# Kernel optimization log

Measured on AMD Instinct MI355X. Metric: run time of the kernel, lower is better.

Reference implementation:

```python
import jax, jax.numpy as jnp
import numpy as np

B, S, D, H, HD, I, L = 1, 2048, 1024, 16, 64, 2816, 2
EPS = 1e-5
ROPE_BASE = 10000.0


def rmsnorm(x, w):
    return x * jax.lax.rsqrt(jnp.mean(x * x, axis=-1, keepdims=True) + EPS) * w


def precompute_freqs_cis():
    # matches precompute_freqs_cis: [S, HD//2, 2] = (cos, sin)
    freqs = 1.0 / (ROPE_BASE ** (jnp.arange(0, HD, 2, dtype=jnp.float32) / HD))
    ang = jnp.outer(jnp.arange(S, dtype=jnp.float32), freqs)
    return jnp.stack([jnp.cos(ang), jnp.sin(ang)], axis=-1)


def apply_rope(x, fc):
    # x: [B,S,H,HD]; fc: [S,HD//2,2] -> interleaved pair rotation
    xs = x.reshape(*x.shape[:-1], HD // 2, 2)
    f = fc[None, :, None]  # [1,S,1,HD//2,2]
    out = jnp.stack([
        xs[..., 0] * f[..., 0] - xs[..., 1] * f[..., 1],
        xs[..., 1] * f[..., 0] + xs[..., 0] * f[..., 1],
    ], axis=-1)
    return out.reshape(x.shape)


def setup_inputs() -> dict:
    key = jax.random.key(0)
    ks = jax.random.split(key, 6)
    p = lambda k, shape: jax.random.normal(k, shape, jnp.float32) * 0.02
    return {
        "x": jax.random.normal(ks[0], (B, S, D), jnp.float32),
        "wqkv": p(ks[1], (L, 3 * H * HD, D)),
        "wo": p(ks[2], (L, D, H * HD)),
        "w1": p(ks[3], (L, I, D)),
        "w2": p(ks[4], (L, D, I)),
        "w3": p(ks[5], (L, I, D)),
        "attn_norm_w": jnp.ones((L, D), jnp.float32),
        "ffn_norm_w": jnp.ones((L, D), jnp.float32),
        "attn_ls": 0.01 * jnp.ones((L, D), jnp.float32),
        "ffn_ls": 0.01 * jnp.ones((L, D), jnp.float32),
        "final_norm_w": jnp.ones((D,), jnp.float32),
    }


def reference(x, wqkv, wo, w1, w2, w3, attn_norm_w, ffn_norm_w, attn_ls, ffn_ls, final_norm_w):
    fc = precompute_freqs_cis()
    causal = jnp.tril(jnp.ones((S, S), dtype=bool))  # [S,S]
    scale = 1.0 / np.sqrt(HD).astype(np.float32)
    h = x
    for l in range(L):
        # --- attention block ---
        xn = rmsnorm(h, attn_norm_w[l])
        qkv = xn @ wqkv[l].T  # [B,S,3*H*HD]
        q, k, v = jnp.split(qkv, 3, axis=-1)
        q = apply_rope(q.reshape(B, S, H, HD), fc)
        k = apply_rope(k.reshape(B, S, H, HD), fc)
        v = v.reshape(B, S, H, HD)
        scores = jnp.einsum('bqhd,bkhd->bhqk', q, k) * scale
        scores = jnp.where(causal, scores, jnp.finfo(scores.dtype).min)
        attn = jax.nn.softmax(scores, axis=-1)
        y = jnp.einsum('bhqk,bkhd->bqhd', attn, v).reshape(B, S, H * HD)
        h = h + (y @ wo[l].T) * attn_ls[l]
        # --- feed-forward block (SwiGLU) ---
        xn = rmsnorm(h, ffn_norm_w[l])
        ff = (jax.nn.silu(xn @ w1[l].T) * (xn @ w3[l].T)) @ w2[l].T
        h = h + ff * ffn_ls[l]
    return rmsnorm(h, final_norm_w)
```

## Files before the change

### kernel.cpp

```cpp
#include <hip/hip_runtime.h>
#include <math.h>

#define SEQ 2048
#define DIM 1024
#define NH 16
#define HDIM 64
#define IDIM 2816
#define NL 2

typedef __attribute__((ext_vector_type(8))) short bf16x8;
typedef __attribute__((ext_vector_type(4))) float f32x4;

__device__ __forceinline__ unsigned short f2bf(float f) {
    unsigned int u = __float_as_uint(f);
    u = (u + 0x7fffu + ((u >> 16) & 1u)) >> 16;
    return (unsigned short)u;
}
__device__ __forceinline__ float bf2f(unsigned short u) {
    return __uint_as_float((unsigned int)u << 16);
}

__device__ __forceinline__ void gl_lds16(const void* g, void* l) {
    __builtin_amdgcn_global_load_lds(
        (const __attribute__((address_space(1))) unsigned int*)g,
        (__attribute__((address_space(3))) unsigned int*)l, 16, 0, 0);
}

#define WAITVM(n) asm volatile("s_waitcnt vmcnt(" #n ")" ::: "memory")
#define BARRIER_PIN()                       \
    do {                                    \
        __builtin_amdgcn_s_barrier();       \
        __builtin_amdgcn_sched_barrier(0);  \
    } while (0)

template <bool BF16OUT>
__global__ __launch_bounds__(256) void rmsnorm_kernel(const float* __restrict__ in,
                                                      const float* __restrict__ w,
                                                      void* __restrict__ out) {
    const int row = blockIdx.x;
    const int t = threadIdx.x;
    const float4 v = ((const float4*)(in + (size_t)row * DIM))[t];
    float ss = v.x * v.x + v.y * v.y + v.z * v.z + v.w * v.w;
#pragma unroll
    for (int m = 1; m < 64; m <<= 1) ss += __shfl_xor(ss, m);
    __shared__ float red[4];
    if ((t & 63) == 0) red[t >> 6] = ss;
    __syncthreads();
    const float tot = red[0] + red[1] + red[2] + red[3];
    const float r = 1.0f / sqrtf(tot * (1.0f / DIM) + 1e-5f);
    const float4 wv = ((const float4*)w)[t];
    float o0 = v.x * r * wv.x, o1 = v.y * r * wv.y;
    float o2 = v.z * r * wv.z, o3 = v.w * r * wv.w;
    if (BF16OUT) {
        ushort4 o = {f2bf(o0), f2bf(o1), f2bf(o2), f2bf(o3)};
        ((ushort4*)((unsigned short*)out + (size_t)row * DIM))[t] = o;
    } else {
        float4 o = {o0, o1, o2, o3};
        ((float4*)((float*)out + (size_t)row * DIM))[t] = o;
    }
}

#define WQKV_OFF 0
#define WO_OFF   3145728
#define W1_OFF   4194304
#define W3_OFF   7077888
#define W2_OFF   9961472
#define WTOT     12845056

__global__ __launch_bounds__(256) void convert_weights_kernel(
    const float* __restrict__ wqkv, const float* __restrict__ wo,
    const float* __restrict__ w1, const float* __restrict__ w3,
    const float* __restrict__ w2, unsigned short* __restrict__ out) {
    const size_t i8 = ((size_t)blockIdx.x * 256 + threadIdx.x) * 8;
    const float* src;
    size_t local;
    if (i8 < WO_OFF)      { src = wqkv; local = i8 - WQKV_OFF; }
    else if (i8 < W1_OFF) { src = wo;   local = i8 - WO_OFF; }
    else if (i8 < W3_OFF) { src = w1;   local = i8 - W1_OFF; }
    else if (i8 < W2_OFF) { src = w3;   local = i8 - W3_OFF; }
    else                  { src = w2;   local = i8 - W2_OFF; }
    const float4 v0 = *(const float4*)(src + local);
    const float4 v1 = *(const float4*)(src + local + 4);
    ushort4 o0 = {f2bf(v0.x), f2bf(v0.y), f2bf(v0.z), f2bf(v0.w)};
    ushort4 o1 = {f2bf(v1.x), f2bf(v1.y), f2bf(v1.z), f2bf(v1.w)};
    *(ushort4*)(out + i8) = o0;
    *(ushort4*)(out + i8 + 4) = o1;
}

template <int EPI, int BM, int BN, int KSPLIT>
__global__ __launch_bounds__(256) void mfma_gemm(
    const unsigned short* __restrict__ A,
    const unsigned short* __restrict__ B,
    const unsigned short* __restrict__ Bhi, int nsplit,
    float* __restrict__ Cf,
    unsigned short* __restrict__ Cb,
    const float* __restrict__ ls,
    int N, int K) {
    constexpr int MI = BM / 32;
    constexpr int NJ = BN / 32;
    constexpr int L = (BM + BN) / 32;
    static_assert(L == 6 || L == 8, "WAITVM literals cover L=6,8");
    __shared__ unsigned short As[2][BM * 64];
    __shared__ unsigned short Bs[2][BN * 64];

    const int tid = threadIdx.x;

    const int nwg = gridDim.x * gridDim.y;
    const int orig = blockIdx.y * gridDim.x + blockIdx.x;
    const int swz = (orig & 7) * (nwg >> 3) + (orig >> 3);
    const int bx = swz % gridDim.x;
    const int by = swz / gridDim.x;
    const int m0 = by * BM;
    const int ncol0 = bx * BN;

    const unsigned short* Bp = B;
    int n0 = ncol0;
    if (n0 >= nsplit) { Bp = Bhi; n0 -= nsplit; }

    const int Koff = (KSPLIT > 1) ? blockIdx.z * (K / KSPLIT) : 0;

    const int r0 = tid >> 3;
    const int cswz = (tid & 7) ^ (r0 & 7);
    const unsigned short* Ag = A + (size_t)(m0 + r0) * K + Koff + cswz * 8;
    const unsigned short* Bg = Bp + (size_t)(n0 + r0) * K + Koff + cswz * 8;

    const int lane = tid & 63;
    const int wid = tid >> 6;
    const int wr = (wid >> 1) * (BM / 2);
    const int wc = (wid & 1) * (BN / 2);
    const int fr = lane & 15;
    const int hi = lane >> 4;

    f32x4 acc[MI][NJ] = {};

    auto stage = [&](int buf, int kk) {
#pragma unroll
        for (int q = 0; q < BM / 32; ++q)
            gl_lds16(Ag + (size_t)(q * 32) * K + kk, &As[buf][q * 2048 + tid * 8]);
#pragma unroll
        for (int q = 0; q < BN / 32; ++q)
            gl_lds16(Bg + (size_t)(q * 32) * K + kk, &Bs[buf][q * 2048 + tid * 8]);
    };

    auto frag = [&](const unsigned short* base, int R, int c) -> bf16x8 {
        return *(const bf16x8*)&base[R * 64 + ((c ^ (R & 7)) << 3)];
    };

    auto compute_tile = [&](int buf) {
        bf16x8 a[MI][2], b[NJ][2];
#pragma unroll
        for (int m = 0; m < MI; ++m)
#pragma unroll
            for (int kw = 0; kw < 2; ++kw)
                a[m][kw] = frag(As[buf], wr + m * 16 + fr, kw * 4 + hi);
#pragma unroll
        for (int n = 0; n < NJ; ++n)
#pragma unroll
            for (int kw = 0; kw < 2; ++kw)
                b[n][kw] = frag(Bs[buf], wc + n * 16 + fr, kw * 4 + hi);
        __builtin_amdgcn_s_setprio(1);
#pragma unroll
        for (int kw = 0; kw < 2; ++kw)
#pragma unroll
            for (int m = 0; m < MI; ++m)
#pragma unroll
                for (int n = 0; n < NJ; ++n)
                    acc[m][n] = __builtin_amdgcn_mfma_f32_16x16x32_bf16(
                        a[m][kw], b[n][kw], acc[m][n], 0, 0, 0);
        __builtin_amdgcn_s_setprio(0);
    };

    const int NT = K / KSPLIT / 64;

    stage(0, 0);
    stage(1, 64);

    int buf = 0;
    for (int t = 0; t < NT - 1; ++t) {
        if constexpr (L == 6) WAITVM(6); else WAITVM(8);
        BARRIER_PIN();
        compute_tile(buf);
        asm volatile("s_waitcnt lgkmcnt(0)" ::: "memory");
        BARRIER_PIN();
        if (t + 2 < NT) stage(buf, (t + 2) * 64);
        buf ^= 1;
    }
    WAITVM(0);
    BARRIER_PIN();
    compute_tile(buf);

    const int erow = m0 + wr + hi * 4;
    const int ecol = ncol0 + wc + fr;
#pragma unroll
    for (int m = 0; m < MI; ++m) {
#pragma unroll
        for (int n = 0; n < NJ; ++n) {
            const f32x4 v = acc[m][n];
            const int row = erow + m * 16;
            const int col = ecol + n * 16;
            if (EPI == 1) {
                const float lv = ls[col];
#pragma unroll
                for (int j = 0; j < 4; ++j) {
                    float* p = Cf + (size_t)(row + j) * N + col;
                    if (KSPLIT > 1) atomicAdd(p, v[j] * lv);
                    else            *p = *p + v[j] * lv;
                }
            } else {
#pragma unroll
                for (int j = 0; j < 4; ++j)
                    Cb[(size_t)(row + j) * N + col] = f2bf(v[j]);
            }
        }
    }
}

__global__ __launch_bounds__(256) void silu_mul_kernel(
    const unsigned short* __restrict__ c13,
    unsigned short* __restrict__ outp) {
    const size_t e8 = ((size_t)blockIdx.x * 256 + threadIdx.x) * 8;
    const int m = (int)(e8 / IDIM);
    const int i = (int)(e8 % IDIM);
    const unsigned short* g = c13 + (size_t)m * (2 * IDIM) + i;
    const bf16x8 gv = *(const bf16x8*)g;
    const bf16x8 uv = *(const bf16x8*)(g + IDIM);
    unsigned short o[8];
#pragma unroll
    for (int j = 0; j < 8; ++j) {
        const float x = bf2f((unsigned short)gv[j]);
        const float u = bf2f((unsigned short)uv[j]);
        o[j] = f2bf(x / (1.0f + __expf(-x)) * u);
    }
    *(bf16x8*)(outp + (size_t)m * IDIM + i) = *(const bf16x8*)o;
}

__global__ __launch_bounds__(256) void rope_split_kernel(
    const unsigned short* __restrict__ qkv,
    unsigned short* __restrict__ Qh,
    unsigned short* __restrict__ Kh,
    unsigned short* __restrict__ Vt) {
    const int st = blockIdx.x;
    const int h = blockIdx.y;
    const int tid = threadIdx.x;
    const int srow = tid >> 2;
    const int scol = (tid & 3) * 16;
    const int s = st * 64 + srow;
    __shared__ unsigned short Vl[64][72];

    const unsigned short* base = qkv + (size_t)s * (3 * DIM) + h * HDIM + scol;

    unsigned short qv[16], kv[16], vv[16];
    *(bf16x8*)&qv[0] = *(const bf16x8*)(base);
    *(bf16x8*)&qv[8] = *(const bf16x8*)(base + 8);
    *(bf16x8*)&kv[0] = *(const bf16x8*)(base + DIM);
    *(bf16x8*)&kv[8] = *(const bf16x8*)(base + DIM + 8);
    *(bf16x8*)&vv[0] = *(const bf16x8*)(base + 2 * DIM);
    *(bf16x8*)&vv[8] = *(const bf16x8*)(base + 2 * DIM + 8);

    unsigned short qo[16], ko[16];
#pragma unroll
    for (int i = 0; i < 8; ++i) {
        const int p = scol / 2 + i;
        const float freq = powf(10000.0f, -(float)(2 * p) * (1.0f / 64.0f));
        const float ang = (float)s * freq;
        float sn, cs;
        sincosf(ang, &sn, &cs);
        const float q0 = bf2f(qv[2 * i]), q1 = bf2f(qv[2 * i + 1]);
        const float k0 = bf2f(kv[2 * i]), k1 = bf2f(kv[2 * i + 1]);
        qo[2 * i]     = f2bf(q0 * cs - q1 * sn);
        qo[2 * i + 1] = f2bf(q1 * cs + q0 * sn);
        ko[2 * i]     = f2bf(k0 * cs - k1 * sn);
        ko[2 * i + 1] = f2bf(k1 * cs + k0 * sn);
    }
    unsigned short* qdst = Qh + ((size_t)h * SEQ + s) * HDIM + scol;
    unsigned short* kdst = Kh + ((size_t)h * SEQ + s) * HDIM + scol;
    *(bf16x8*)qdst = *(const bf16x8*)&qo[0];
    *(bf16x8*)(qdst + 8) = *(const bf16x8*)&qo[8];
    *(bf16x8*)kdst = *(const bf16x8*)&ko[0];
    *(bf16x8*)(kdst + 8) = *(const bf16x8*)&ko[8];

#pragma unroll
    for (int i = 0; i < 16; ++i) Vl[scol + i][srow] = vv[i];
    __syncthreads();
    const int d = tid >> 2;
    const int c0 = (tid & 3) * 16;
    unsigned short* vdst = Vt + ((size_t)h * HDIM + d) * SEQ + st * 64 + c0;
    *(bf16x8*)vdst = *(const bf16x8*)&Vl[d][c0];
    *(bf16x8*)(vdst + 8) = *(const bf16x8*)&Vl[d][c0 + 8];
}

__global__ __launch_bounds__(256) void attn_mfma_kernel(
    const unsigned short* __restrict__ Qh,
    const unsigned short* __restrict__ Kh,
    const unsigned short* __restrict__ Vt,
    unsigned short* __restrict__ y) {
    const int h = blockIdx.x;
    const int qt = blockIdx.y;
    const int qb = (qt < 16) ? qt : 47 - qt;

    __shared__ unsigned short Ql[64][72];
    __shared__ unsigned short Kl[2][64][72];
    __shared__ unsigned short Vl[2][64][72];
    __shared__ unsigned short Pl[64][72];

    const int tid = threadIdx.x;
    const int lane = tid & 63;
    const int w = tid >> 6;
    const int fr = lane & 15;
    const int fk = (lane >> 4) * 8;
    const int rg = (lane >> 4) * 4;
    const int srow = tid >> 2;
    const int sc8 = (tid & 3) * 8;

    {
        const unsigned short* src = Qh + ((size_t)h * SEQ + qb * 64 + srow) * HDIM + sc8;
        *(bf16x8*)&Ql[srow][sc8] = *(const bf16x8*)src;
        *(bf16x8*)&Ql[srow][sc8 + 32] = *(const bf16x8*)(src + 32);
    }
    __syncthreads();
    bf16x8 qa[2];
    qa[0] = *(const bf16x8*)&Ql[w * 16 + fr][fk];
    qa[1] = *(const bf16x8*)&Ql[w * 16 + fr][32 + fk];

    bf16x8 kr0, kr1, vr0, vr1;
    {
        const unsigned short* ks = Kh + ((size_t)h * SEQ + srow) * HDIM + sc8;
        kr0 = *(const bf16x8*)ks;
        kr1 = *(const bf16x8*)(ks + 32);
        const unsigned short* vs = Vt + ((size_t)h * HDIM + srow) * SEQ + sc8;
        vr0 = *(const bf16x8*)vs;
        vr1 = *(const bf16x8*)(vs + 32);
    }

    float l_[4] = {0.0f, 0.0f, 0.0f, 0.0f};
    f32x4 O[4] = {};

    for (int kb = 0; kb <= qb; ++kb) {
        const int cur = kb & 1;
        *(bf16x8*)&Kl[cur][srow][sc8] = kr0;
        *(bf16x8*)&Kl[cur][srow][sc8 + 32] = kr1;
        *(bf16x8*)&Vl[cur][srow][sc8] = vr0;
        *(bf16x8*)&Vl[cur][srow][sc8 + 32] = vr1;
        __syncthreads();

        if (kb < qb) {
            const unsigned short* ks = Kh + ((size_t)h * SEQ + (kb + 1) * 64 + srow) * HDIM + sc8;
            kr0 = *(const bf16x8*)ks;
            kr1 = *(const bf16x8*)(ks + 32);
            const unsigned short* vs = Vt + ((size_t)h * HDIM + srow) * SEQ + (kb + 1) * 64 + sc8;
            vr0 = *(const bf16x8*)vs;
            vr1 = *(const bf16x8*)(vs + 32);
        }

        f32x4 sa[4] = {};
        __builtin_amdgcn_s_setprio(1);
#pragma unroll
        for (int ks2 = 0; ks2 < 2; ++ks2)
#pragma unroll
            for (int n = 0; n < 4; ++n) {
                const bf16x8 kf = *(const bf16x8*)&Kl[cur][n * 16 + fr][ks2 * 32 + fk];
                sa[n] = __builtin_amdgcn_mfma_f32_16x16x32_bf16(qa[ks2], kf, sa[n], 0, 0, 0);
            }
        __builtin_amdgcn_s_setprio(0);

        const bool diag = (kb == qb);
#pragma unroll
        for (int n = 0; n < 4; ++n) {
            const int col = n * 16 + fr;
#pragma unroll
            for (int j = 0; j < 4; ++j) {
                const float sv = sa[n][j] * 0.125f;
                float e = __expf(fminf(sv, 30.0f));
                if (diag && col > rg + j) e = 0.0f;
                l_[j] += e;
                Pl[w * 16 + rg + j][col] = f2bf(e);
            }
        }

        __builtin_amdgcn_s_setprio(1);
#pragma unroll
        for (int ks2 = 0; ks2 < 2; ++ks2) {
            const bf16x8 pa = *(const bf16x8*)&Pl[w * 16 + fr][ks2 * 32 + fk];
#pragma unroll
            for (int nd = 0; nd < 4; ++nd) {
                const bf16x8 vf = *(const bf16x8*)&Vl[cur][nd * 16 + fr][ks2 * 32 + fk];
                O[nd] = __builtin_amdgcn_mfma_f32_16x16x32_bf16(pa, vf, O[nd], 0, 0, 0);
            }
        }
        __builtin_amdgcn_s_setprio(0);
    }

#pragma unroll
    for (int j = 0; j < 4; ++j) {
#pragma unroll
        for (int msk = 1; msk < 16; msk <<= 1) l_[j] += __shfl_xor(l_[j], msk);
    }

#pragma unroll
    for (int j = 0; j < 4; ++j) {
        const float inv = 1.0f / l_[j];
        unsigned short* dst = y + (size_t)(qb * 64 + w * 16 + rg + j) * DIM + h * HDIM + fr;
#pragma unroll
        for (int nd = 0; nd < 4; ++nd)
            dst[nd * 16] = f2bf(O[nd][j] * inv);
    }
}

extern "C" void kernel_launch(void* const* d_in, const int* in_sizes, int n_in,
                              void* d_out, int out_size, void* d_ws, size_t ws_size,
                              hipStream_t stream) {
    const float* x            = (const float*)d_in[0];
    const float* wqkv         = (const float*)d_in[1];
    const float* wo           = (const float*)d_in[2];
    const float* w1           = (const float*)d_in[3];
    const float* w2           = (const float*)d_in[4];
    const float* w3           = (const float*)d_in[5];
    const float* attn_norm_w  = (const float*)d_in[6];
    const float* ffn_norm_w   = (const float*)d_in[7];
    const float* attn_ls      = (const float*)d_in[8];
    const float* ffn_ls       = (const float*)d_in[9];
    const float* final_norm_w = (const float*)d_in[10];
    float* out = (float*)d_out;

    char* ws = (char*)d_ws;
    float*          h     = (float*)ws;
    unsigned short* xnb   = (unsigned short*)(ws + 8388608);
    unsigned short* yb    = (unsigned short*)(ws + 12582912);
    unsigned short* qkvb  = (unsigned short*)(ws + 16777216);
    unsigned short* Qhb   = (unsigned short*)(ws + 29360128);
    unsigned short* Khb   = (unsigned short*)(ws + 33554432);
    unsigned short* Vtb   = (unsigned short*)(ws + 37748736);
    unsigned short* c13   = (unsigned short*)(ws + 16777216);
    unsigned short* ffb   = (unsigned short*)(ws + 41943040);
    unsigned short* wbuf  = (unsigned short*)(ws + 46137344);

    unsigned short* wqkv_b = wbuf + WQKV_OFF;
    unsigned short* wo_b   = wbuf + WO_OFF;
    unsigned short* w1_b   = wbuf + W1_OFF;
    unsigned short* w3_b   = wbuf + W3_OFF;
    unsigned short* w2_b   = wbuf + W2_OFF;

    const int BIG = 1 << 30;

    hipMemcpyAsync(h, x, (size_t)SEQ * DIM * sizeof(float),
                   hipMemcpyDeviceToDevice, stream);

    for (int l = 0; l < NL; ++l) {
        convert_weights_kernel<<<WTOT / 2048, 256, 0, stream>>>(
            wqkv + (size_t)l * 3 * DIM * DIM, wo + (size_t)l * DIM * DIM,
            w1 + (size_t)l * IDIM * DIM, w3 + (size_t)l * IDIM * DIM,
            w2 + (size_t)l * DIM * IDIM, wbuf);

        rmsnorm_kernel<true><<<SEQ, 256, 0, stream>>>(h, attn_norm_w + l * DIM, xnb);
        mfma_gemm<3, 128, 128, 1><<<dim3(3 * DIM / 128, SEQ / 128), 256, 0, stream>>>(
            xnb, wqkv_b, nullptr, BIG, nullptr, qkvb, nullptr, 3 * DIM, DIM);
        rope_split_kernel<<<dim3(SEQ / 64, NH), 256, 0, stream>>>(qkvb, Qhb, Khb, Vtb);
        attn_mfma_kernel<<<dim3(NH, SEQ / 64), 256, 0, stream>>>(Qhb, Khb, Vtb, yb);
        mfma_gemm<1, 64, 128, 2><<<dim3(DIM / 128, SEQ / 64, 2), 256, 0, stream>>>(
            yb, wo_b, nullptr, BIG, h, nullptr, attn_ls + l * DIM, DIM, DIM);

        rmsnorm_kernel<true><<<SEQ, 256, 0, stream>>>(h, ffn_norm_w + l * DIM, xnb);
        mfma_gemm<3, 128, 128, 1><<<dim3(2 * IDIM / 128, SEQ / 128), 256, 0, stream>>>(
            xnb, w1_b, w3_b, IDIM, nullptr, c13, nullptr, 2 * IDIM, DIM);
        silu_mul_kernel<<<SEQ * IDIM / 2048, 256, 0, stream>>>(c13, ffb);
        mfma_gemm<1, 128, 128, 4><<<dim3(DIM / 128, SEQ / 128, 4), 256, 0, stream>>>(
            ffb, w2_b, nullptr, BIG, h, nullptr, ffn_ls + l * DIM, DIM, IDIM);
    }

    rmsnorm_kernel<false><<<SEQ, 256, 0, stream>>>(h, final_norm_w, out);
}
```

Before: 376.5 us.

## Process 128-key tiles per attention iteration and swap GEMM tile raster order

```diff
diff --git a/kernel.cpp b/kernel.cpp
--- a/kernel.cpp
+++ b/kernel.cpp
@@ -108,8 +108,8 @@
     const int nwg = gridDim.x * gridDim.y;
     const int orig = blockIdx.y * gridDim.x + blockIdx.x;
     const int swz = (orig & 7) * (nwg >> 3) + (orig >> 3);
-    const int bx = swz % gridDim.x;
-    const int by = swz / gridDim.x;
+    const int bx = swz / gridDim.y;
+    const int by = swz % gridDim.y;
     const int m0 = by * BM;
     const int ncol0 = bx * BN;
 
@@ -257,11 +257,12 @@
     *(bf16x8*)&vv[0] = *(const bf16x8*)(base + 2 * DIM);
     *(bf16x8*)&vv[8] = *(const bf16x8*)(base + 2 * DIM + 8);
 
+    const float FC = -0.28782313662425572f;
     unsigned short qo[16], ko[16];
 #pragma unroll
     for (int i = 0; i < 8; ++i) {
         const int p = scol / 2 + i;
-        const float freq = powf(10000.0f, -(float)(2 * p) * (1.0f / 64.0f));
+        const float freq = __expf(FC * (float)p);
         const float ang = (float)s * freq;
         float sn, cs;
         sincosf(ang, &sn, &cs);
@@ -299,9 +300,9 @@
     const int qb = (qt < 16) ? qt : 47 - qt;
 
     __shared__ unsigned short Ql[64][72];
-    __shared__ unsigned short Kl[2][64][72];
-    __shared__ unsigned short Vl[2][64][72];
-    __shared__ unsigned short Pl[64][72];
+    __shared__ unsigned short Kl[128][72];
+    __shared__ unsigned short Vl[64][136];
+    __shared__ unsigned short Pl[64][136];
 
     const int tid = threadIdx.x;
     const int lane = tid & 63;
@@ -309,81 +310,91 @@
     const int fr = lane & 15;
     const int fk = (lane >> 4) * 8;
     const int rg = (lane >> 4) * 4;
-    const int srow = tid >> 2;
-    const int sc8 = (tid & 3) * 8;
 
     {
-        const unsigned short* src = Qh + ((size_t)h * SEQ + qb * 64 + srow) * HDIM + sc8;
-        *(bf16x8*)&Ql[srow][sc8] = *(const bf16x8*)src;
-        *(bf16x8*)&Ql[srow][sc8 + 32] = *(const bf16x8*)(src + 32);
+        const int qr = tid >> 2, qc = (tid & 3) * 16;
+        const unsigned short* src = Qh + ((size_t)h * SEQ + qb * 64 + qr) * HDIM + qc;
+        *(bf16x8*)&Ql[qr][qc] = *(const bf16x8*)src;
+        *(bf16x8*)&Ql[qr][qc + 8] = *(const bf16x8*)(src + 8);
     }
     __syncthreads();
     bf16x8 qa[2];
     qa[0] = *(const bf16x8*)&Ql[w * 16 + fr][fk];
     qa[1] = *(const bf16x8*)&Ql[w * 16 + fr][32 + fk];
 
-    bf16x8 kr0, kr1, vr0, vr1;
+    const int krow = tid >> 1, kc0 = (tid & 1) * 32;
+    const int vd = tid >> 2, vc0 = (tid & 3) * 32;
+
+    const int nst = qb / 2 + 1;
+
+    bf16x8 kr[4], vr[4];
     {
-        const unsigned short* ks = Kh + ((size_t)h * SEQ + srow) * HDIM + sc8;
-        kr0 = *(const bf16x8*)ks;
-        kr1 = *(const bf16x8*)(ks + 32);
-        const unsigned short* vs = Vt + ((size_t)h * HDIM + srow) * SEQ + sc8;
-        vr0 = *(const bf16x8*)vs;
-        vr1 = *(const bf16x8*)(vs + 32);
+        const unsigned short* ks = Kh + ((size_t)h * SEQ + krow) * HDIM + kc0;
+        kr[0] = *(const bf16x8*)(ks);      kr[1] = *(const bf16x8*)(ks + 8);
+        kr[2] = *(const bf16x8*)(ks + 16); kr[3] = *(const bf16x8*)(ks + 24);
+        const unsigned short* vs = Vt + ((size_t)h * HDIM + vd) * SEQ + vc0;
+        vr[0] = *(const bf16x8*)(vs);      vr[1] = *(const bf16x8*)(vs + 8);
+        vr[2] = *(const bf16x8*)(vs + 16); vr[3] = *(const bf16x8*)(vs + 24);
     }
 
     float l_[4] = {0.0f, 0.0f, 0.0f, 0.0f};
     f32x4 O[4] = {};
 
-    for (int kb = 0; kb <= qb; ++kb) {
-        const int cur = kb & 1;
-        *(bf16x8*)&Kl[cur][srow][sc8] = kr0;
-        *(bf16x8*)&Kl[cur][srow][sc8 + 32] = kr1;
-        *(bf16x8*)&Vl[cur][srow][sc8] = vr0;
-        *(bf16x8*)&Vl[cur][srow][sc8 + 32] = vr1;
+    for (int st = 0; st < nst; ++st) {
+        if (st > 0) __syncthreads();
+        *(bf16x8*)&Kl[krow][kc0]      = kr[0];
+        *(bf16x8*)&Kl[krow][kc0 + 8]  = kr[1];
+        *(bf16x8*)&Kl[krow][kc0 + 16] = kr[2];
+        *(bf16x8*)&Kl[krow][kc0 + 24] = kr[3];
+        *(bf16x8*)&Vl[vd][vc0]      = vr[0];
+        *(bf16x8*)&Vl[vd][vc0 + 8]  = vr[1];
+        *(bf16x8*)&Vl[vd][vc0 + 16] = vr[2];
+        *(bf16x8*)&Vl[vd][vc0 + 24] = vr[3];
         __syncthreads();
 
-        if (kb < qb) {
-            const unsigned short* ks = Kh + ((size_t)h * SEQ + (kb + 1) * 64 + srow) * HDIM + sc8;
-            kr0 = *(const bf16x8*)ks;
-            kr1 = *(const bf16x8*)(ks + 32);
-            const unsigned short* vs = Vt + ((size_t)h * HDIM + srow) * SEQ + (kb + 1) * 64 + sc8;
-            vr0 = *(const bf16x8*)vs;
-            vr1 = *(const bf16x8*)(vs + 32);
+        if (st + 1 < nst) {
+            const unsigned short* ks =
+                Kh + ((size_t)h * SEQ + (st + 1) * 128 + krow) * HDIM + kc0;
+            kr[0] = *(const bf16x8*)(ks);      kr[1] = *(const bf16x8*)(ks + 8);
+            kr[2] = *(const bf16x8*)(ks + 16); kr[3] = *(const bf16x8*)(ks + 24);
+            const unsigned short* vs =
+                Vt + ((size_t)h * HDIM + vd) * SEQ + (st + 1) * 128 + vc0;
+            vr[0] = *(const bf16x8*)(vs);      vr[1] = *(const bf16x8*)(vs + 8);
+            vr[2] = *(const bf16x8*)(vs + 16); vr[3] = *(const bf16x8*)(vs + 24);
         }
 
-        f32x4 sa[4] = {};
+        f32x4 sa[8] = {};
         __builtin_amdgcn_s_setprio(1);
 #pragma unroll
-        for (int ks2 = 0; ks2 < 2; ++ks2)
-#pragma unroll
-            for (int n = 0; n < 4; ++n) {
-                const bf16x8 kf = *(const bf16x8*)&Kl[cur][n * 16 + fr][ks2 * 32 + fk];
-                sa[n] = __builtin_amdgcn_mfma_f32_16x16x32_bf16(qa[ks2], kf, sa[n], 0, 0, 0);
+        for (int kw = 0; kw < 2; ++kw)
+#pragma unroll
+            for (int c = 0; c < 8; ++c) {
+                const bf16x8 kf = *(const bf16x8*)&Kl[c * 16 + fr][kw * 32 + fk];
+                sa[c] = __builtin_amdgcn_mfma_f32_16x16x32_bf16(qa[kw], kf, sa[c], 0, 0, 0);
             }
         __builtin_amdgcn_s_setprio(0);
 
-        const bool diag = (kb == qb);
-#pragma unroll
-        for (int n = 0; n < 4; ++n) {
-            const int col = n * 16 + fr;
+        const bool lastst = (st == nst - 1);
+#pragma unroll
+        for (int c = 0; c < 8; ++c) {
+            const int col = st * 128 + c * 16 + fr;
 #pragma unroll
             for (int j = 0; j < 4; ++j) {
-                const float sv = sa[n][j] * 0.125f;
+                const float sv = sa[c][j] * 0.125f;
                 float e = __expf(fminf(sv, 30.0f));
-                if (diag && col > rg + j) e = 0.0f;
+                if (lastst && col > (qb * 64 + w * 16 + rg + j)) e = 0.0f;
                 l_[j] += e;
-                Pl[w * 16 + rg + j][col] = f2bf(e);
+                Pl[w * 16 + rg + j][c * 16 + fr] = f2bf(e);
             }
         }
 
         __builtin_amdgcn_s_setprio(1);
 #pragma unroll
-        for (int ks2 = 0; ks2 < 2; ++ks2) {
+        for (int ks2 = 0; ks2 < 4; ++ks2) {
             const bf16x8 pa = *(const bf16x8*)&Pl[w * 16 + fr][ks2 * 32 + fk];
 #pragma unroll
             for (int nd = 0; nd < 4; ++nd) {
-                const bf16x8 vf = *(const bf16x8*)&Vl[cur][nd * 16 + fr][ks2 * 32 + fk];
+                const bf16x8 vf = *(const bf16x8*)&Vl[nd * 16 + fr][ks2 * 32 + fk];
                 O[nd] = __builtin_amdgcn_mfma_f32_16x16x32_bf16(pa, vf, O[nd], 0, 0, 0);
             }
         }
```

New measurement: 383.9 us. Within noise of the previous version (+2.0%).
